# Kernel optimization log

Hardware: AMD Instinct MI355X
Metric: run time of the kernel (lower is better)

## Reference

```python
import jax, jax.numpy as jnp
import numpy as np

N, D, C, S, E, K, MIN_MATCH, N_ITER = 100000, 128, 16, 16, 3200000, 64, 1, 4


def setup_inputs() -> dict:
    key = jax.random.key(0)
    k1, k2, k3, k4 = jax.random.split(key, 4)
    es = jax.random.normal(k1, (N, D), jnp.float32)
    edge_index = jax.random.randint(k2, (2, E), 0, N)
    seeds = jax.random.randint(k3, (C, S), 0, N)
    W = jax.random.normal(k4, (D, D), jnp.float32) / np.float32(np.sqrt(D))
    return {"es": es, "edge_index": edge_index, "seeds": seeds, "W": W, "n_iter": N_ITER}


def _memory_step(es, idx, hx, W):
    # ragged gather of last expansion, padded to fixed size per class: [C, k, D]
    inp = es[idx]
    d = inp.shape[-1]
    q = jnp.mean(inp, axis=1) if hx is None else hx          # attention query [C, D]
    logits = jnp.einsum('ckd,cd->ck', inp, q) / jnp.sqrt(jnp.float32(d))
    a = jax.nn.softmax(logits, axis=-1)                      # [C, k]
    ctx = jnp.einsum('ck,ckd->cd', a, inp)                   # attended read [C, D]
    pre = ctx if hx is None else ctx + hx                    # recurrent memory update
    return jnp.tanh(pre @ W)                                 # [C, D]


def _cosine(x, y):
    xn = x / (jnp.linalg.norm(x, axis=-1, keepdims=True) + 1e-8)
    yn = y / (jnp.linalg.norm(y, axis=-1, keepdims=True) + 1e-8)
    return xn @ yn.T                                         # [N, C]


def _expand(es, W, edge_index, seeds, n_iter):
    n, c = es.shape[0], seeds.shape[0]
    src, dst = edge_index[0], edge_index[1]
    # known_mask.scatter_(0, seed_all, 1)
    known = jnp.zeros((n,), bool).at[seeds.ravel()].set(True)
    # get_cate_mask(seeds, N): per-class membership mask [C, N]
    cate = jnp.zeros((c, n), bool).at[jnp.arange(c)[:, None], seeds].set(True)
    hx, last = None, seeds
    outs, exps, hxes = [], [], []
    for _ in range(n_iter):
        hx = _memory_step(es, last, hx, W)
        # get_cate_neighbors: per-class count of in-edges whose source is in the class
        counts = jax.vmap(lambda m: jax.ops.segment_sum(m, dst, num_segments=n))(
            cate.astype(jnp.float32)[:, src])                # [C, N]
        valid = (counts >= MIN_MATCH) & (~known)[None, :]    # [C, N]
        scores = _cosine(es, hx).T                           # [C, N]
        # _select: top n_expansion valid nodes per class (finite fill avoids -inf grads)
        probs, idx = jax.lax.top_k(jnp.where(valid, scores, -1e9), K)
        known = known.at[idx.ravel()].set(True)
        cate = cate.at[jnp.arange(c)[:, None], idx].set(True)
        last = idx
        outs.append(probs); exps.append(idx); hxes.append(hx)
    return jnp.stack(outs), jnp.stack(exps), jnp.stack(hxes)


def reference(es, edge_index, seeds, W, n_iter):
    return _expand(es, W, edge_index, seeds, n_iter)
```

## Files before the change

kernel.cpp:

```cpp
#include <hip/hip_runtime.h>
#include <math.h>

#define NN 100000
#define DD 128
#define CC 16
#define SS 16
#define EE 3200000
#define KK 64
#define NIT 4
#define CNT_STRIDE 32
#define NB 32
#define SLMAX 4096
#define MM (NB * KK)
#define EB ((EE + 255) / 256)
#define INF_STAMP 0x7fffffff

typedef unsigned long long ull;

__device__ inline ull ordkey(double d) {
    long long b = __double_as_longlong(d);
    return (b < 0) ? ~(ull)b : ((ull)b | 0x8000000000000000ULL);
}
__device__ inline double keyord(ull u) {
    long long b = (u & 0x8000000000000000ULL)
                    ? (long long)(u & 0x7FFFFFFFFFFFFFFFULL)
                    : (long long)~u;
    return __longlong_as_double(b);
}
__device__ inline bool gt(ull ka, int na, ull kb, int nb) {
    return (ka > kb) || (ka == kb && na < nb);
}

__device__ inline void wsort64(ull& k, int& n, int lane) {
    for (int k2 = 2; k2 <= 64; k2 <<= 1) {
        for (int j = k2 >> 1; j; j >>= 1) {
            ull ok = __shfl_xor(k, j, 64);
            int on = __shfl_xor(n, j, 64);
            bool isLow = (lane & j) == 0;
            bool d = (k2 == 64) || ((lane & k2) == 0);
            bool wantMax = (d == isLow);
            if (wantMax == gt(ok, on, k, n)) { k = ok; n = on; }
        }
    }
}
__device__ inline void wmerge64(ull& k, int& n, int lane) {
    for (int j = 32; j; j >>= 1) {
        ull ok = __shfl_xor(k, j, 64);
        int on = __shfl_xor(n, j, 64);
        bool wantMax = (lane & j) == 0;
        if (wantMax == gt(ok, on, k, n)) { k = ok; n = on; }
    }
}


__global__ __launch_bounds__(256)
void k_init(const float* __restrict__ es, double* __restrict__ inv_norm,
            int* __restrict__ known, unsigned* __restrict__ cate,
            unsigned* __restrict__ nbr) {
    int wave = threadIdx.x >> 6, lane = threadIdx.x & 63;
    int n = blockIdx.x * 4 + wave;
    if (n >= NN) return;
    float a = es[(long)n * DD + lane];
    float b = es[(long)n * DD + 64 + lane];
    double p = (double)a * (double)a + (double)b * (double)b;
    for (int o = 32; o > 0; o >>= 1) p += __shfl_xor(p, o, 64);
    if (lane == 0) {
        inv_norm[n] = 1.0 / (sqrt(p) + 1e-8);
        known[n] = INF_STAMP;
        cate[n] = 0;
        nbr[n] = 0;
    }
}

__global__ void k_seed(const int* __restrict__ seeds, int* __restrict__ known,
                       unsigned* __restrict__ cate) {
    int i = threadIdx.x;
    if (i < CC * SS) {
        int n = seeds[i];
        known[n] = 0;
        atomicOr(&cate[n], 1u << (i / SS));
    }
}


__global__ __launch_bounds__(256)
void k_memedge(const float* __restrict__ es, const float* __restrict__ Wm,
               const int* __restrict__ seeds, const int* __restrict__ last,
               double* __restrict__ hx, double* __restrict__ hxn,
               float* __restrict__ out, int* __restrict__ cnt,
               const int* __restrict__ edge, const unsigned* __restrict__ cate,
               unsigned* __restrict__ nbr, int t) {
    __shared__ float  inp[KK][DD + 1];
    __shared__ int    rowS[KK];
    __shared__ double q[DD];
    __shared__ double lg[KK];
    __shared__ double sr[KK];
    __shared__ double pre[DD];
    __shared__ double red[DD];
    int tid = threadIdx.x;

    if (blockIdx.x >= CC) {
        long e = (long)(blockIdx.x - CC) * 256 + tid;
        if (e < EE) {
            int s = edge[e];
            unsigned m = cate[s];
            if (m) {
                int d = edge[EE + e];
                atomicOr(&nbr[d], m);
            }
        }
        return;
    }

    int c = blockIdx.x;
    if (tid == 0) cnt[c * CNT_STRIDE] = 0;
    int k = (t == 0) ? SS : KK;
    if (tid < KK) {
        lg[tid] = -1.0e308;
        if (tid < k) rowS[tid] = (t == 0) ? seeds[c * SS + tid] : last[c * KK + tid];
    }
    __syncthreads();
    for (int i = tid; i < k * DD; i += 256)
        inp[i >> 7][i & 127] = es[(long)rowS[i >> 7] * DD + (i & 127)];
    __syncthreads();
    if (tid < DD) {
        if (t == 0) {
            double s = 0;
            for (int j = 0; j < k; ++j) s += (double)inp[j][tid];
            q[tid] = s / (double)k;
        } else {
            q[tid] = hx[c * DD + tid];
        }
    }
    __syncthreads();
    if (tid < k) {
        double s = 0;
        for (int i = 0; i < DD; ++i) s += (double)inp[tid][i] * q[i];
        lg[tid] = s / sqrt((double)DD);
    }
    __syncthreads();
    if (tid < KK) sr[tid] = lg[tid];
    __syncthreads();
    for (int st = 32; st > 0; st >>= 1) {
        if (tid < st) sr[tid] = fmax(sr[tid], sr[tid + st]);
        __syncthreads();
    }
    double mx = sr[0];
    __syncthreads();
    if (tid < KK) {
        double e = (tid < k) ? exp(lg[tid] - mx) : 0.0;
        lg[tid] = e; sr[tid] = e;
    }
    __syncthreads();
    for (int st = 32; st > 0; st >>= 1) {
        if (tid < st) sr[tid] += sr[tid + st];
        __syncthreads();
    }
    double sm = sr[0];
    __syncthreads();
    if (tid < KK) lg[tid] /= sm;
    __syncthreads();
    if (tid < DD) {
        double ctx = 0;
        for (int j = 0; j < k; ++j) ctx += lg[j] * (double)inp[j][tid];
        pre[tid] = (t == 0) ? ctx : (ctx + q[tid]);
    }
    __syncthreads();
    double h = 0;
    if (tid < DD) {
        for (int i = 0; i < DD; ++i) h += pre[i] * (double)Wm[i * DD + tid];
        h = tanh(h);
        red[tid] = h * h;
    }
    __syncthreads();
    for (int st = 64; st > 0; st >>= 1) {
        if (tid < st) red[tid] += red[tid + st];
        __syncthreads();
    }
    if (tid < DD) {
        double inv = 1.0 / (sqrt(red[0]) + 1e-8);
        hx[c * DD + tid] = h;
        hxn[c * DD + tid] = h * inv;
        out[2 * NIT * CC * KK + t * CC * DD + c * DD + tid] = (float)h;
    }
}


__global__ __launch_bounds__(256)
void k_cand(const float* __restrict__ es, const double* __restrict__ inv_norm,
            const int* __restrict__ known, const unsigned* __restrict__ nbr,
            const double* __restrict__ hxn,
            int* __restrict__ cnt, int* __restrict__ cidx,
            ull* __restrict__ ckey, int cap, int t) {
    __shared__ int    pair[256 * 16];
    __shared__ short  prank[256 * 16];
    __shared__ double hxnL[CC * 129];
    __shared__ int    lcnt[CC];
    __shared__ int    base[CC];
    __shared__ int    npair;
    int tid = threadIdx.x;

    for (int i = tid; i < CC * DD; i += 256)
        hxnL[(i >> 7) * 129 + (i & 127)] = hxn[i];
    if (tid < CC) lcnt[tid] = 0;
    if (tid == 0) npair = 0;
    __syncthreads();

    int n = blockIdx.x * 256 + tid;
    unsigned m = 0;
    if (n < NN && known[n] > t) m = nbr[n];
    while (m) {
        int c = __ffs(m) - 1;
        m &= m - 1;
        int r = atomicAdd(&lcnt[c], 1);
        int p = atomicAdd(&npair, 1);
        pair[p] = (n << 4) | c;
        prank[p] = (short)r;
    }
    __syncthreads();

    if (tid < CC && lcnt[tid] > 0)
        base[tid] = atomicAdd(&cnt[tid * CNT_STRIDE], lcnt[tid]);
    __syncthreads();

    int np = npair;
    for (int t2 = tid; t2 < np; t2 += 256) {
        int pk = pair[t2];
        int nn = pk >> 4, c = pk & 15;
        const float4* row = (const float4*)(es + (long)nn * DD);
        const double* h = &hxnL[c * 129];
        double s = 0;
        #pragma unroll
        for (int i = 0; i < 32; ++i) {
            float4 v = row[i];
            s += (double)v.x * h[4 * i + 0] + (double)v.y * h[4 * i + 1]
               + (double)v.z * h[4 * i + 2] + (double)v.w * h[4 * i + 3];
        }
        int pos = base[c] + (int)prank[t2];
        if (pos < cap) {
            cidx[(long)c * cap + pos] = nn;
            ckey[(long)c * cap + pos] = ordkey(s * inv_norm[nn]);
        }
    }
}


__global__ __launch_bounds__(256)
void k_top(const int* __restrict__ cnt, const int* __restrict__ cidx,
           const ull* __restrict__ ckey, int cap,
           ull* __restrict__ tkey, int* __restrict__ tnode) {
    __shared__ ull ks[SLMAX];
    __shared__ int ns[SLMAX];
    int c = blockIdx.x / NB, b = blockIdx.x % NB;
    int tid = threadIdx.x, wave = tid >> 6, lane = tid & 63;
    int count = min(cnt[c * CNT_STRIDE], cap);
    int per = (count + NB - 1) / NB;
    int start = b * per;
    int m = min(per, count - start);
    int sl = 64;
    while (sl < per) sl <<= 1;
    int nruns = sl >> 6;
    for (int r = wave; r < nruns; r += 4) {
        int i = (r << 6) + lane;
        ull k; int n;
        if (i < m) { k = ckey[(long)c * cap + start + i]; n = cidx[(long)c * cap + start + i]; }
        else       { k = 0ULL; n = 0x7FFFFFFF; }
        wsort64(k, n, lane);
        ks[i] = k; ns[i] = n;
    }
    __syncthreads();
    for (int step = 1; step < nruns; step <<= 1) {
        int npair2 = nruns / (2 * step);
        for (int pr = wave; pr < npair2; pr += 4) {
            int ra = pr * 2 * step, rb = ra + step;
            ull ka = ks[(ra << 6) + lane];       int na = ns[(ra << 6) + lane];
            ull kb = ks[(rb << 6) + 63 - lane];  int nb2 = ns[(rb << 6) + 63 - lane];
            if (gt(kb, nb2, ka, na)) { ka = kb; na = nb2; }
            wmerge64(ka, na, lane);
            ks[(ra << 6) + lane] = ka; ns[(ra << 6) + lane] = na;
        }
        __syncthreads();
    }
    if (tid < KK) {
        tkey[(long)c * MM + b * KK + tid] = ks[tid];
        tnode[(long)c * MM + b * KK + tid] = ns[tid];
    }
}


__global__ __launch_bounds__(256)
void k_mergeupd(const int* __restrict__ cnt,
                const ull* __restrict__ tkey, const int* __restrict__ tnode,
                int* __restrict__ known, const unsigned* __restrict__ nbr,
                unsigned* __restrict__ cate, int* __restrict__ last,
                float* __restrict__ out, int cap, int t) {
    __shared__ ull ks[MM];
    __shared__ int ns[MM];
    int c = blockIdx.x, tid = threadIdx.x, wave = tid >> 6, lane = tid & 63;
    for (int i = tid; i < MM; i += 256) {
        ks[i] = tkey[(long)c * MM + i];
        ns[i] = tnode[(long)c * MM + i];
    }
    __syncthreads();
    for (int step = 1; step < NB; step <<= 1) {
        int npair2 = NB / (2 * step);
        for (int pr = wave; pr < npair2; pr += 4) {
            int ra = pr * 2 * step, rb = ra + step;
            ull ka = ks[(ra << 6) + lane];       int na = ns[(ra << 6) + lane];
            ull kb = ks[(rb << 6) + 63 - lane];  int nb2 = ns[(rb << 6) + 63 - lane];
            if (gt(kb, nb2, ka, na)) { ka = kb; na = nb2; }
            wmerge64(ka, na, lane);
            ks[(ra << 6) + lane] = ka; ns[(ra << 6) + lane] = na;
        }
        __syncthreads();
    }
    int count = min(cnt[c * CNT_STRIDE], cap);
    int nsel = min(count, KK);
    if (tid < KK && tid < nsel) {
        int n = ns[tid];
        out[t * CC * KK + c * KK + tid] = (float)keyord(ks[tid]);
        out[NIT * CC * KK + t * CC * KK + c * KK + tid] = (float)n;
        last[c * KK + tid] = n;
        known[n] = t + 1;
        atomicOr(&cate[n], 1u << c);
    }
    if (tid == 0 && nsel < KK) {
        int r = nsel;
        for (int n = 0; n < NN && r < KK; ++n) {
            bool valid = ((nbr[n] >> c) & 1u) && (known[n] > t);
            if (!valid) {
                out[t * CC * KK + c * KK + r] = -1e9f;
                out[NIT * CC * KK + t * CC * KK + c * KK + r] = (float)n;
                last[c * KK + r] = n;
                known[n] = t + 1;
                atomicOr(&cate[n], 1u << c);
                ++r;
            }
        }
    }
}


extern "C" void kernel_launch(void* const* d_in, const int* in_sizes, int n_in,
                              void* d_out, int out_size, void* d_ws, size_t ws_size,
                              hipStream_t stream) {
    const float* es    = (const float*)d_in[0];
    const int*   edge  = (const int*)d_in[1];
    const int*   seeds = (const int*)d_in[2];
    const float* W     = (const float*)d_in[3];
    float* out = (float*)d_out;

    char* p = (char*)d_ws;
    auto alloc = [&](size_t bytes) -> char* {
        char* r = p;
        p += (bytes + 255) & ~(size_t)255;
        return r;
    };
    double*   inv_norm = (double*)alloc((size_t)NN * 8);
    int*      known    = (int*)alloc((size_t)NN * 4);
    unsigned* cate     = (unsigned*)alloc((size_t)NN * 4);
    unsigned* nbr      = (unsigned*)alloc((size_t)NN * 4);
    double*   hx       = (double*)alloc(CC * DD * 8);
    double*   hxn      = (double*)alloc(CC * DD * 8);
    int*      last     = (int*)alloc(CC * KK * 4);
    int*      cnt      = (int*)alloc(CC * CNT_STRIDE * 4);
    ull*      tkey     = (ull*)alloc((size_t)CC * MM * 8);
    int*      tnode    = (int*)alloc((size_t)CC * MM * 4);
    size_t used = (size_t)(p - (char*)d_ws);
    size_t rem = (ws_size > used + 8192) ? (ws_size - used - 8192) : 0;
    long capl = (long)(rem / (CC * 12));
    if (capl > NN) capl = NN;
    if (capl < 1) capl = 1;
    int cap = (int)capl;
    int*    cidx = (int*)alloc((size_t)CC * cap * 4);
    ull*    ckey = (ull*)alloc((size_t)CC * cap * 8);

    k_init<<<(NN + 3) / 4, 256, 0, stream>>>(es, inv_norm, known, cate, nbr);
    k_seed<<<1, 256, 0, stream>>>(seeds, known, cate);

    for (int t = 0; t < NIT; ++t) {
        k_memedge<<<CC + EB, 256, 0, stream>>>(es, W, seeds, last, hx, hxn, out,
                                               cnt, edge, cate, nbr, t);
        k_cand<<<(NN + 255) / 256, 256, 0, stream>>>(es, inv_norm, known, nbr, hxn,
                                                     cnt, cidx, ckey, cap, t);
        k_top<<<CC * NB, 256, 0, stream>>>(cnt, cidx, ckey, cap, tkey, tnode);
        k_mergeupd<<<CC, 256, 0, stream>>>(cnt, tkey, tnode, known, nbr,
                                           cate, last, out, cap, t);
    }
}
```

Before: 308.4 us.

## Fuse all stages into one persistent kernel with software grid barriers

Replaces the per-iteration sequence of memory/edge, candidate, top-k and merge kernels with a single persistent kernel of 256 blocks that synchronises via an atomic generation-counter grid barrier. Init and seeding are merged into one pass that checks seed membership from shared memory. This removes many kernel launches and launch gaps. In exchange, it runs bandwidth-heavy edge and candidate passes with only one block per CU, which may reduce latency hiding, and it relies on all blocks being co-resident.

```diff
diff --git a/kernel.cpp b/kernel.cpp
--- a/kernel.cpp
+++ b/kernel.cpp
@@ -12,10 +12,30 @@
 #define NB 32
 #define SLMAX 4096
 #define MM (NB * KK)
-#define EB ((EE + 255) / 256)
+#define GRID 256
+#define NCHUNK ((NN + 255) / 256)
 #define INF_STAMP 0x7fffffff
 
 typedef unsigned long long ull;
+
+__device__ int g_cnt = 0;
+__device__ int g_gen = 0;
+
+__device__ __forceinline__ void gridbar() {
+    __syncthreads();
+    if (threadIdx.x == 0) {
+        int g = __hip_atomic_load(&g_gen, __ATOMIC_RELAXED, __HIP_MEMORY_SCOPE_AGENT);
+        int a = __hip_atomic_fetch_add(&g_cnt, 1, __ATOMIC_ACQ_REL, __HIP_MEMORY_SCOPE_AGENT);
+        if (a == GRID - 1) {
+            __hip_atomic_store(&g_cnt, 0, __ATOMIC_RELAXED, __HIP_MEMORY_SCOPE_AGENT);
+            __hip_atomic_fetch_add(&g_gen, 1, __ATOMIC_RELEASE, __HIP_MEMORY_SCOPE_AGENT);
+        } else {
+            while (__hip_atomic_load(&g_gen, __ATOMIC_ACQUIRE, __HIP_MEMORY_SCOPE_AGENT) == g)
+                __builtin_amdgcn_s_sleep(1);
+        }
+    }
+    __syncthreads();
+}
 
 __device__ inline ull ordkey(double d) {
     long long b = __double_as_longlong(d);
@@ -52,291 +72,273 @@
     }
 }
 
-
-__global__ __launch_bounds__(256)
-void k_init(const float* __restrict__ es, double* __restrict__ inv_norm,
-            int* __restrict__ known, unsigned* __restrict__ cate,
-            unsigned* __restrict__ nbr) {
-    int wave = threadIdx.x >> 6, lane = threadIdx.x & 63;
-    int n = blockIdx.x * 4 + wave;
-    if (n >= NN) return;
-    float a = es[(long)n * DD + lane];
-    float b = es[(long)n * DD + 64 + lane];
-    double p = (double)a * (double)a + (double)b * (double)b;
-    for (int o = 32; o > 0; o >>= 1) p += __shfl_xor(p, o, 64);
-    if (lane == 0) {
-        inv_norm[n] = 1.0 / (sqrt(p) + 1e-8);
-        known[n] = INF_STAMP;
-        cate[n] = 0;
-        nbr[n] = 0;
-    }
-}
-
-__global__ void k_seed(const int* __restrict__ seeds, int* __restrict__ known,
-                       unsigned* __restrict__ cate) {
-    int i = threadIdx.x;
-    if (i < CC * SS) {
-        int n = seeds[i];
-        known[n] = 0;
-        atomicOr(&cate[n], 1u << (i / SS));
-    }
-}
-
-
-__global__ __launch_bounds__(256)
-void k_memedge(const float* __restrict__ es, const float* __restrict__ Wm,
-               const int* __restrict__ seeds, const int* __restrict__ last,
-               double* __restrict__ hx, double* __restrict__ hxn,
-               float* __restrict__ out, int* __restrict__ cnt,
-               const int* __restrict__ edge, const unsigned* __restrict__ cate,
-               unsigned* __restrict__ nbr, int t) {
-    __shared__ float  inp[KK][DD + 1];
-    __shared__ int    rowS[KK];
-    __shared__ double q[DD];
-    __shared__ double lg[KK];
-    __shared__ double sr[KK];
-    __shared__ double pre[DD];
-    __shared__ double red[DD];
-    int tid = threadIdx.x;
-
-    if (blockIdx.x >= CC) {
-        long e = (long)(blockIdx.x - CC) * 256 + tid;
-        if (e < EE) {
-            int s = edge[e];
-            unsigned m = cate[s];
-            if (m) {
-                int d = edge[EE + e];
-                atomicOr(&nbr[d], m);
-            }
-        }
-        return;
-    }
-
-    int c = blockIdx.x;
-    if (tid == 0) cnt[c * CNT_STRIDE] = 0;
-    int k = (t == 0) ? SS : KK;
-    if (tid < KK) {
-        lg[tid] = -1.0e308;
-        if (tid < k) rowS[tid] = (t == 0) ? seeds[c * SS + tid] : last[c * KK + tid];
-    }
+union SMem {
+    struct {
+        float inp[KK][DD + 1];
+        int rowS[KK];
+        double q[DD], lg[KK], sr[KK], pre[DD], red[DD];
+    } m;
+    struct {
+        int pair[256 * 16];
+        short prank[256 * 16];
+        double hxnL[CC * 129];
+        int lcnt[CC], base[CC], npair;
+    } cd;
+    struct { ull ks[SLMAX]; int ns[SLMAX]; } tp;
+    struct { int sn[CC * SS]; } sd;
+};
+
+__global__ __launch_bounds__(256, 1)
+void k_all(const float* __restrict__ es, const int* __restrict__ edge,
+           const int* __restrict__ seeds, const float* __restrict__ Wm,
+           float* __restrict__ out,
+           double* __restrict__ inv_norm, int* __restrict__ known,
+           unsigned* __restrict__ cate, unsigned* __restrict__ nbr,
+           double* __restrict__ hx, double* __restrict__ hxn,
+           int* __restrict__ last, int* __restrict__ cnt,
+           ull* __restrict__ tkey, int* __restrict__ tnode,
+           int* __restrict__ cidx, ull* __restrict__ ckey, int cap) {
+    __shared__ SMem sm;
+    int tid = threadIdx.x, wave = tid >> 6, lane = tid & 63;
+
+    if (tid < CC * SS) sm.sd.sn[tid] = seeds[tid];
     __syncthreads();
-    for (int i = tid; i < k * DD; i += 256)
-        inp[i >> 7][i & 127] = es[(long)rowS[i >> 7] * DD + (i & 127)];
-    __syncthreads();
-    if (tid < DD) {
-        if (t == 0) {
-            double s = 0;
-            for (int j = 0; j < k; ++j) s += (double)inp[j][tid];
-            q[tid] = s / (double)k;
+    for (int n = blockIdx.x * 4 + wave; n < NN; n += GRID * 4) {
+        float a = es[(long)n * DD + lane];
+        float b = es[(long)n * DD + 64 + lane];
+        double p = (double)a * (double)a + (double)b * (double)b;
+        for (int o = 32; o > 0; o >>= 1) p += __shfl_xor(p, o, 64);
+        unsigned bits = 0;
+        #pragma unroll
+        for (int j = 0; j < 4; ++j) {
+            int idx = lane * 4 + j;
+            if (sm.sd.sn[idx] == n) bits |= 1u << (idx >> 4);
+        }
+        for (int o = 32; o > 0; o >>= 1) bits |= __shfl_xor(bits, o, 64);
+        if (lane == 0) {
+            inv_norm[n] = 1.0 / (sqrt(p) + 1e-8);
+            known[n] = bits ? 0 : INF_STAMP;
+            cate[n] = bits;
+            nbr[n] = 0;
+        }
+    }
+    gridbar();
+
+    for (int t = 0; t < NIT; ++t) {
+        if (blockIdx.x < CC) {
+            int c = blockIdx.x;
+            if (tid == 0) cnt[c * CNT_STRIDE] = 0;
+            int k = (t == 0) ? SS : KK;
+            if (tid < KK) {
+                sm.m.lg[tid] = -1.0e308;
+                if (tid < k) sm.m.rowS[tid] = (t == 0) ? seeds[c * SS + tid]
+                                                       : last[c * KK + tid];
+            }
+            __syncthreads();
+            for (int i = tid; i < k * DD; i += 256)
+                sm.m.inp[i >> 7][i & 127] = es[(long)sm.m.rowS[i >> 7] * DD + (i & 127)];
+            __syncthreads();
+            if (tid < DD) {
+                if (t == 0) {
+                    double s = 0;
+                    for (int j = 0; j < k; ++j) s += (double)sm.m.inp[j][tid];
+                    sm.m.q[tid] = s / (double)k;
+                } else {
+                    sm.m.q[tid] = hx[c * DD + tid];
+                }
+            }
+            __syncthreads();
+            if (tid < k) {
+                double s = 0;
+                for (int i = 0; i < DD; ++i) s += (double)sm.m.inp[tid][i] * sm.m.q[i];
+                sm.m.lg[tid] = s / sqrt((double)DD);
+            }
+            __syncthreads();
+            if (tid < KK) sm.m.sr[tid] = sm.m.lg[tid];
+            __syncthreads();
+            for (int st = 32; st > 0; st >>= 1) {
+                if (tid < st) sm.m.sr[tid] = fmax(sm.m.sr[tid], sm.m.sr[tid + st]);
+                __syncthreads();
+            }
+            double mx = sm.m.sr[0];
+            __syncthreads();
+            if (tid < KK) {
+                double e = (tid < k) ? exp(sm.m.lg[tid] - mx) : 0.0;
+                sm.m.lg[tid] = e; sm.m.sr[tid] = e;
+            }
+            __syncthreads();
+            for (int st = 32; st > 0; st >>= 1) {
+                if (tid < st) sm.m.sr[tid] += sm.m.sr[tid + st];
+                __syncthreads();
+            }
+            double smm = sm.m.sr[0];
+            __syncthreads();
+            if (tid < KK) sm.m.lg[tid] /= smm;
+            __syncthreads();
+            if (tid < DD) {
+                double ctx = 0;
+                for (int j = 0; j < k; ++j) ctx += sm.m.lg[j] * (double)sm.m.inp[j][tid];
+                sm.m.pre[tid] = (t == 0) ? ctx : (ctx + sm.m.q[tid]);
+            }
+            __syncthreads();
+            double h = 0;
+            if (tid < DD) {
+                for (int i = 0; i < DD; ++i) h += sm.m.pre[i] * (double)Wm[i * DD + tid];
+                h = tanh(h);
+                sm.m.red[tid] = h * h;
+            }
+            __syncthreads();
+            for (int st = 64; st > 0; st >>= 1) {
+                if (tid < st) sm.m.red[tid] += sm.m.red[tid + st];
+                __syncthreads();
+            }
+            if (tid < DD) {
+                double inv = 1.0 / (sqrt(sm.m.red[0]) + 1e-8);
+                hx[c * DD + tid] = h;
+                hxn[c * DD + tid] = h * inv;
+                out[2 * NIT * CC * KK + t * CC * DD + c * DD + tid] = (float)h;
+            }
         } else {
-            q[tid] = hx[c * DD + tid];
-        }
-    }
-    __syncthreads();
-    if (tid < k) {
-        double s = 0;
-        for (int i = 0; i < DD; ++i) s += (double)inp[tid][i] * q[i];
-        lg[tid] = s / sqrt((double)DD);
-    }
-    __syncthreads();
-    if (tid < KK) sr[tid] = lg[tid];
-    __syncthreads();
-    for (int st = 32; st > 0; st >>= 1) {
-        if (tid < st) sr[tid] = fmax(sr[tid], sr[tid + st]);
+            const int stripe = (EE + (GRID - CC) - 1) / (GRID - CC);
+            long e0 = (long)(blockIdx.x - CC) * stripe;
+            long e1 = e0 + stripe; if (e1 > EE) e1 = EE;
+            for (long e = e0 + tid; e < e1; e += 256) {
+                int s = edge[e];
+                unsigned mm = cate[s];
+                if (mm) atomicOr(&nbr[edge[EE + e]], mm);
+            }
+        }
+        gridbar();
+
+        for (int i = tid; i < CC * DD; i += 256)
+            sm.cd.hxnL[(i >> 7) * 129 + (i & 127)] = hxn[i];
         __syncthreads();
-    }
-    double mx = sr[0];
-    __syncthreads();
-    if (tid < KK) {
-        double e = (tid < k) ? exp(lg[tid] - mx) : 0.0;
-        lg[tid] = e; sr[tid] = e;
-    }
-    __syncthreads();
-    for (int st = 32; st > 0; st >>= 1) {
-        if (tid < st) sr[tid] += sr[tid + st];
-        __syncthreads();
-    }
-    double sm = sr[0];
-    __syncthreads();
-    if (tid < KK) lg[tid] /= sm;
-    __syncthreads();
-    if (tid < DD) {
-        double ctx = 0;
-        for (int j = 0; j < k; ++j) ctx += lg[j] * (double)inp[j][tid];
-        pre[tid] = (t == 0) ? ctx : (ctx + q[tid]);
-    }
-    __syncthreads();
-    double h = 0;
-    if (tid < DD) {
-        for (int i = 0; i < DD; ++i) h += pre[i] * (double)Wm[i * DD + tid];
-        h = tanh(h);
-        red[tid] = h * h;
-    }
-    __syncthreads();
-    for (int st = 64; st > 0; st >>= 1) {
-        if (tid < st) red[tid] += red[tid + st];
-        __syncthreads();
-    }
-    if (tid < DD) {
-        double inv = 1.0 / (sqrt(red[0]) + 1e-8);
-        hx[c * DD + tid] = h;
-        hxn[c * DD + tid] = h * inv;
-        out[2 * NIT * CC * KK + t * CC * DD + c * DD + tid] = (float)h;
-    }
-}
-
-
-__global__ __launch_bounds__(256)
-void k_cand(const float* __restrict__ es, const double* __restrict__ inv_norm,
-            const int* __restrict__ known, const unsigned* __restrict__ nbr,
-            const double* __restrict__ hxn,
-            int* __restrict__ cnt, int* __restrict__ cidx,
-            ull* __restrict__ ckey, int cap, int t) {
-    __shared__ int    pair[256 * 16];
-    __shared__ short  prank[256 * 16];
-    __shared__ double hxnL[CC * 129];
-    __shared__ int    lcnt[CC];
-    __shared__ int    base[CC];
-    __shared__ int    npair;
-    int tid = threadIdx.x;
-
-    for (int i = tid; i < CC * DD; i += 256)
-        hxnL[(i >> 7) * 129 + (i & 127)] = hxn[i];
-    if (tid < CC) lcnt[tid] = 0;
-    if (tid == 0) npair = 0;
-    __syncthreads();
-
-    int n = blockIdx.x * 256 + tid;
-    unsigned m = 0;
-    if (n < NN && known[n] > t) m = nbr[n];
-    while (m) {
-        int c = __ffs(m) - 1;
-        m &= m - 1;
-        int r = atomicAdd(&lcnt[c], 1);
-        int p = atomicAdd(&npair, 1);
-        pair[p] = (n << 4) | c;
-        prank[p] = (short)r;
-    }
-    __syncthreads();
-
-    if (tid < CC && lcnt[tid] > 0)
-        base[tid] = atomicAdd(&cnt[tid * CNT_STRIDE], lcnt[tid]);
-    __syncthreads();
-
-    int np = npair;
-    for (int t2 = tid; t2 < np; t2 += 256) {
-        int pk = pair[t2];
-        int nn = pk >> 4, c = pk & 15;
-        const float4* row = (const float4*)(es + (long)nn * DD);
-        const double* h = &hxnL[c * 129];
-        double s = 0;
-        #pragma unroll
-        for (int i = 0; i < 32; ++i) {
-            float4 v = row[i];
-            s += (double)v.x * h[4 * i + 0] + (double)v.y * h[4 * i + 1]
-               + (double)v.z * h[4 * i + 2] + (double)v.w * h[4 * i + 3];
-        }
-        int pos = base[c] + (int)prank[t2];
-        if (pos < cap) {
-            cidx[(long)c * cap + pos] = nn;
-            ckey[(long)c * cap + pos] = ordkey(s * inv_norm[nn]);
-        }
-    }
-}
-
-
-__global__ __launch_bounds__(256)
-void k_top(const int* __restrict__ cnt, const int* __restrict__ cidx,
-           const ull* __restrict__ ckey, int cap,
-           ull* __restrict__ tkey, int* __restrict__ tnode) {
-    __shared__ ull ks[SLMAX];
-    __shared__ int ns[SLMAX];
-    int c = blockIdx.x / NB, b = blockIdx.x % NB;
-    int tid = threadIdx.x, wave = tid >> 6, lane = tid & 63;
-    int count = min(cnt[c * CNT_STRIDE], cap);
-    int per = (count + NB - 1) / NB;
-    int start = b * per;
-    int m = min(per, count - start);
-    int sl = 64;
-    while (sl < per) sl <<= 1;
-    int nruns = sl >> 6;
-    for (int r = wave; r < nruns; r += 4) {
-        int i = (r << 6) + lane;
-        ull k; int n;
-        if (i < m) { k = ckey[(long)c * cap + start + i]; n = cidx[(long)c * cap + start + i]; }
-        else       { k = 0ULL; n = 0x7FFFFFFF; }
-        wsort64(k, n, lane);
-        ks[i] = k; ns[i] = n;
-    }
-    __syncthreads();
-    for (int step = 1; step < nruns; step <<= 1) {
-        int npair2 = nruns / (2 * step);
-        for (int pr = wave; pr < npair2; pr += 4) {
-            int ra = pr * 2 * step, rb = ra + step;
-            ull ka = ks[(ra << 6) + lane];       int na = ns[(ra << 6) + lane];
-            ull kb = ks[(rb << 6) + 63 - lane];  int nb2 = ns[(rb << 6) + 63 - lane];
-            if (gt(kb, nb2, ka, na)) { ka = kb; na = nb2; }
-            wmerge64(ka, na, lane);
-            ks[(ra << 6) + lane] = ka; ns[(ra << 6) + lane] = na;
-        }
-        __syncthreads();
-    }
-    if (tid < KK) {
-        tkey[(long)c * MM + b * KK + tid] = ks[tid];
-        tnode[(long)c * MM + b * KK + tid] = ns[tid];
-    }
-}
-
-
-__global__ __launch_bounds__(256)
-void k_mergeupd(const int* __restrict__ cnt,
-                const ull* __restrict__ tkey, const int* __restrict__ tnode,
-                int* __restrict__ known, const unsigned* __restrict__ nbr,
-                unsigned* __restrict__ cate, int* __restrict__ last,
-                float* __restrict__ out, int cap, int t) {
-    __shared__ ull ks[MM];
-    __shared__ int ns[MM];
-    int c = blockIdx.x, tid = threadIdx.x, wave = tid >> 6, lane = tid & 63;
-    for (int i = tid; i < MM; i += 256) {
-        ks[i] = tkey[(long)c * MM + i];
-        ns[i] = tnode[(long)c * MM + i];
-    }
-    __syncthreads();
-    for (int step = 1; step < NB; step <<= 1) {
-        int npair2 = NB / (2 * step);
-        for (int pr = wave; pr < npair2; pr += 4) {
-            int ra = pr * 2 * step, rb = ra + step;
-            ull ka = ks[(ra << 6) + lane];       int na = ns[(ra << 6) + lane];
-            ull kb = ks[(rb << 6) + 63 - lane];  int nb2 = ns[(rb << 6) + 63 - lane];
-            if (gt(kb, nb2, ka, na)) { ka = kb; na = nb2; }
-            wmerge64(ka, na, lane);
-            ks[(ra << 6) + lane] = ka; ns[(ra << 6) + lane] = na;
-        }
-        __syncthreads();
-    }
-    int count = min(cnt[c * CNT_STRIDE], cap);
-    int nsel = min(count, KK);
-    if (tid < KK && tid < nsel) {
-        int n = ns[tid];
-        out[t * CC * KK + c * KK + tid] = (float)keyord(ks[tid]);
-        out[NIT * CC * KK + t * CC * KK + c * KK + tid] = (float)n;
-        last[c * KK + tid] = n;
-        known[n] = t + 1;
-        atomicOr(&cate[n], 1u << c);
-    }
-    if (tid == 0 && nsel < KK) {
-        int r = nsel;
-        for (int n = 0; n < NN && r < KK; ++n) {
-            bool valid = ((nbr[n] >> c) & 1u) && (known[n] > t);
-            if (!valid) {
-                out[t * CC * KK + c * KK + r] = -1e9f;
-                out[NIT * CC * KK + t * CC * KK + c * KK + r] = (float)n;
-                last[c * KK + r] = n;
+        for (int vb = blockIdx.x; vb < NCHUNK; vb += GRID) {
+            if (tid < CC) sm.cd.lcnt[tid] = 0;
+            if (tid == 0) sm.cd.npair = 0;
+            __syncthreads();
+            int n = vb * 256 + tid;
+            unsigned m = 0;
+            if (n < NN && known[n] > t) m = nbr[n];
+            while (m) {
+                int c = __ffs(m) - 1;
+                m &= m - 1;
+                int r = atomicAdd(&sm.cd.lcnt[c], 1);
+                int p = atomicAdd(&sm.cd.npair, 1);
+                sm.cd.pair[p] = (n << 4) | c;
+                sm.cd.prank[p] = (short)r;
+            }
+            __syncthreads();
+            if (tid < CC && sm.cd.lcnt[tid] > 0)
+                sm.cd.base[tid] = atomicAdd(&cnt[tid * CNT_STRIDE], sm.cd.lcnt[tid]);
+            __syncthreads();
+            int np = sm.cd.npair;
+            for (int t2 = tid; t2 < np; t2 += 256) {
+                int pk = sm.cd.pair[t2];
+                int nn = pk >> 4, c = pk & 15;
+                const float4* row = (const float4*)(es + (long)nn * DD);
+                const double* h = &sm.cd.hxnL[c * 129];
+                double s = 0;
+                #pragma unroll
+                for (int i = 0; i < 32; ++i) {
+                    float4 v = row[i];
+                    s += (double)v.x * h[4 * i + 0] + (double)v.y * h[4 * i + 1]
+                       + (double)v.z * h[4 * i + 2] + (double)v.w * h[4 * i + 3];
+                }
+                int pos = sm.cd.base[c] + (int)sm.cd.prank[t2];
+                if (pos < cap) {
+                    cidx[(long)c * cap + pos] = nn;
+                    ckey[(long)c * cap + pos] = ordkey(s * inv_norm[nn]);
+                }
+            }
+            __syncthreads();
+        }
+        gridbar();
+
+        for (int vt = blockIdx.x; vt < CC * NB; vt += GRID) {
+            int c = vt / NB, b = vt % NB;
+            int count = min(cnt[c * CNT_STRIDE], cap);
+            int per = (count + NB - 1) / NB;
+            int start = b * per;
+            int m2 = min(per, count - start);
+            int sl = 64;
+            while (sl < per) sl <<= 1;
+            int nruns = sl >> 6;
+            __syncthreads();
+            for (int r = wave; r < nruns; r += 4) {
+                int i = (r << 6) + lane;
+                ull k; int n;
+                if (i < m2) { k = ckey[(long)c * cap + start + i];
+                              n = cidx[(long)c * cap + start + i]; }
+                else        { k = 0ULL; n = 0x7FFFFFFF; }
+                wsort64(k, n, lane);
+                sm.tp.ks[i] = k; sm.tp.ns[i] = n;
+            }
+            __syncthreads();
+            for (int step = 1; step < nruns; step <<= 1) {
+                int npair2 = nruns / (2 * step);
+                for (int pr = wave; pr < npair2; pr += 4) {
+                    int ra = pr * 2 * step, rb = ra + step;
+                    ull ka = sm.tp.ks[(ra << 6) + lane];       int na = sm.tp.ns[(ra << 6) + lane];
+                    ull kb = sm.tp.ks[(rb << 6) + 63 - lane];  int nb2 = sm.tp.ns[(rb << 6) + 63 - lane];
+                    if (gt(kb, nb2, ka, na)) { ka = kb; na = nb2; }
+                    wmerge64(ka, na, lane);
+                    sm.tp.ks[(ra << 6) + lane] = ka; sm.tp.ns[(ra << 6) + lane] = na;
+                }
+                __syncthreads();
+            }
+            if (tid < KK) {
+                tkey[(long)c * MM + b * KK + tid] = sm.tp.ks[tid];
+                tnode[(long)c * MM + b * KK + tid] = sm.tp.ns[tid];
+            }
+        }
+        gridbar();
+
+        if (blockIdx.x < CC) {
+            int c = blockIdx.x;
+            for (int i = tid; i < MM; i += 256) {
+                sm.tp.ks[i] = tkey[(long)c * MM + i];
+                sm.tp.ns[i] = tnode[(long)c * MM + i];
+            }
+            __syncthreads();
+            for (int step = 1; step < NB; step <<= 1) {
+                int npair2 = NB / (2 * step);
+                for (int pr = wave; pr < npair2; pr += 4) {
+                    int ra = pr * 2 * step, rb = ra + step;
+                    ull ka = sm.tp.ks[(ra << 6) + lane];       int na = sm.tp.ns[(ra << 6) + lane];
+                    ull kb = sm.tp.ks[(rb << 6) + 63 - lane];  int nb2 = sm.tp.ns[(rb << 6) + 63 - lane];
+                    if (gt(kb, nb2, ka, na)) { ka = kb; na = nb2; }
+                    wmerge64(ka, na, lane);
+                    sm.tp.ks[(ra << 6) + lane] = ka; sm.tp.ns[(ra << 6) + lane] = na;
+                }
+                __syncthreads();
+            }
+            int count = min(cnt[c * CNT_STRIDE], cap);
+            int nsel = min(count, KK);
+            if (tid < KK && tid < nsel) {
+                int n = sm.tp.ns[tid];
+                out[t * CC * KK + c * KK + tid] = (float)keyord(sm.tp.ks[tid]);
+                out[NIT * CC * KK + t * CC * KK + c * KK + tid] = (float)n;
+                last[c * KK + tid] = n;
                 known[n] = t + 1;
                 atomicOr(&cate[n], 1u << c);
-                ++r;
-            }
-        }
+            }
+            if (tid == 0 && nsel < KK) {
+                int r = nsel;
+                for (int n = 0; n < NN && r < KK; ++n) {
+                    bool valid = ((nbr[n] >> c) & 1u) && (known[n] > t);
+                    if (!valid) {
+                        out[t * CC * KK + c * KK + r] = -1e9f;
+                        out[NIT * CC * KK + t * CC * KK + c * KK + r] = (float)n;
+                        last[c * KK + r] = n;
+                        known[n] = t + 1;
+                        atomicOr(&cate[n], 1u << c);
+                        ++r;
+                    }
+                }
+            }
+        }
+        gridbar();
     }
 }
 
@@ -375,16 +377,7 @@
     int*    cidx = (int*)alloc((size_t)CC * cap * 4);
     ull*    ckey = (ull*)alloc((size_t)CC * cap * 8);
 
-    k_init<<<(NN + 3) / 4, 256, 0, stream>>>(es, inv_norm, known, cate, nbr);
-    k_seed<<<1, 256, 0, stream>>>(seeds, known, cate);
-
-    for (int t = 0; t < NIT; ++t) {
-        k_memedge<<<CC + EB, 256, 0, stream>>>(es, W, seeds, last, hx, hxn, out,
-                                               cnt, edge, cate, nbr, t);
-        k_cand<<<(NN + 255) / 256, 256, 0, stream>>>(es, inv_norm, known, nbr, hxn,
-                                                     cnt, cidx, ckey, cap, t);
-        k_top<<<CC * NB, 256, 0, stream>>>(cnt, cidx, ckey, cap, tkey, tnode);
-        k_mergeupd<<<CC, 256, 0, stream>>>(cnt, tkey, tnode, known, nbr,
-                                           cate, last, out, cap, t);
-    }
-}
+    k_all<<<GRID, 256, 0, stream>>>(es, edge, seeds, W, out,
+                                    inv_norm, known, cate, nbr, hx, hxn,
+                                    last, cnt, tkey, tnode, cidx, ckey, cap);
+}
```

Result: slower. 971.0 us (+214.9%).

## Fuse top-k sort and merge into one kernel with last-block-done reduction

Applied to the files above, without the earlier changes.

Replaces the two-kernel top-k (per-block sort into shared memory, then per-class merge kernel) with a single kernel. Each wave streams its slice of candidates and folds them into a running 64-wide top list held in registers. The last block of each class, found through an atomic done counter, does the final fold and the update. Seed initialization is folded into k_init, and the k_cand pair packing drops the separate rank array. This removes kernel launches and large shared-memory sorts, but the final merge is serialized through one wave per class and relies on acq_rel atomic ordering.

```diff
diff --git a/kernel.cpp b/kernel.cpp
--- a/kernel.cpp
+++ b/kernel.cpp
@@ -9,9 +9,9 @@
 #define KK 64
 #define NIT 4
 #define CNT_STRIDE 32
-#define NB 32
-#define SLMAX 4096
-#define MM (NB * KK)
+#define RUNS 64
+#define CHUNK 256
+#define NCH ((NN + CHUNK - 1) / CHUNK)
 #define EB ((EE + 255) / 256)
 #define INF_STAMP 0x7fffffff
 
@@ -51,34 +51,40 @@
         if (wantMax == gt(ok, on, k, n)) { k = ok; n = on; }
     }
 }
+__device__ inline void wfold(ull& ak, int& an, ull k, int n, int lane) {
+    ull rk = __shfl(k, 63 - lane, 64);
+    int rn = __shfl(n, 63 - lane, 64);
+    if (gt(rk, rn, ak, an)) { ak = rk; an = rn; }
+    wmerge64(ak, an, lane);
+}
 
 
 __global__ __launch_bounds__(256)
-void k_init(const float* __restrict__ es, double* __restrict__ inv_norm,
-            int* __restrict__ known, unsigned* __restrict__ cate,
-            unsigned* __restrict__ nbr) {
-    int wave = threadIdx.x >> 6, lane = threadIdx.x & 63;
+void k_init(const float* __restrict__ es, const int* __restrict__ seeds,
+            double* __restrict__ inv_norm, int* __restrict__ known,
+            unsigned* __restrict__ cate, unsigned* __restrict__ nbr) {
+    __shared__ int sn[CC * SS];
+    int tid = threadIdx.x, wave = tid >> 6, lane = tid & 63;
+    if (tid < CC * SS) sn[tid] = seeds[tid];
+    __syncthreads();
     int n = blockIdx.x * 4 + wave;
     if (n >= NN) return;
     float a = es[(long)n * DD + lane];
     float b = es[(long)n * DD + 64 + lane];
     double p = (double)a * (double)a + (double)b * (double)b;
     for (int o = 32; o > 0; o >>= 1) p += __shfl_xor(p, o, 64);
+    unsigned bits = 0;
+    #pragma unroll
+    for (int j = 0; j < 4; ++j) {
+        int idx = lane * 4 + j;
+        if (sn[idx] == n) bits |= 1u << (idx >> 4);
+    }
+    for (int o = 32; o > 0; o >>= 1) bits |= __shfl_xor(bits, o, 64);
     if (lane == 0) {
         inv_norm[n] = 1.0 / (sqrt(p) + 1e-8);
-        known[n] = INF_STAMP;
-        cate[n] = 0;
+        known[n] = bits ? 0 : INF_STAMP;
+        cate[n] = bits;
         nbr[n] = 0;
-    }
-}
-
-__global__ void k_seed(const int* __restrict__ seeds, int* __restrict__ known,
-                       unsigned* __restrict__ cate) {
-    int i = threadIdx.x;
-    if (i < CC * SS) {
-        int n = seeds[i];
-        known[n] = 0;
-        atomicOr(&cate[n], 1u << (i / SS));
     }
 }
 
@@ -87,16 +93,12 @@
 void k_memedge(const float* __restrict__ es, const float* __restrict__ Wm,
                const int* __restrict__ seeds, const int* __restrict__ last,
                double* __restrict__ hx, double* __restrict__ hxn,
-               float* __restrict__ out, int* __restrict__ cnt,
+               float* __restrict__ out, int* __restrict__ cnt, int* __restrict__ done,
                const int* __restrict__ edge, const unsigned* __restrict__ cate,
                unsigned* __restrict__ nbr, int t) {
     __shared__ float  inp[KK][DD + 1];
     __shared__ int    rowS[KK];
-    __shared__ double q[DD];
-    __shared__ double lg[KK];
-    __shared__ double sr[KK];
-    __shared__ double pre[DD];
-    __shared__ double red[DD];
+    __shared__ double q[DD], lg[KK], sr[KK], pre[DD], red[DD];
     int tid = threadIdx.x;
 
     if (blockIdx.x >= CC) {
@@ -104,16 +106,13 @@
         if (e < EE) {
             int s = edge[e];
             unsigned m = cate[s];
-            if (m) {
-                int d = edge[EE + e];
-                atomicOr(&nbr[d], m);
-            }
+            if (m) atomicOr(&nbr[edge[EE + e]], m);
         }
         return;
     }
 
     int c = blockIdx.x;
-    if (tid == 0) cnt[c * CNT_STRIDE] = 0;
+    if (tid == 0) { cnt[c * CNT_STRIDE] = 0; done[c * CNT_STRIDE] = 0; }
     int k = (t == 0) ? SS : KK;
     if (tid < KK) {
         lg[tid] = -1.0e308;
@@ -192,12 +191,9 @@
             const double* __restrict__ hxn,
             int* __restrict__ cnt, int* __restrict__ cidx,
             ull* __restrict__ ckey, int cap, int t) {
-    __shared__ int    pair[256 * 16];
-    __shared__ short  prank[256 * 16];
+    __shared__ int    pair[CHUNK * CC];
     __shared__ double hxnL[CC * 129];
-    __shared__ int    lcnt[CC];
-    __shared__ int    base[CC];
-    __shared__ int    npair;
+    __shared__ int    lcnt[CC], base[CC], npair;
     int tid = threadIdx.x;
 
     for (int i = tid; i < CC * DD; i += 256)
@@ -206,7 +202,7 @@
     if (tid == 0) npair = 0;
     __syncthreads();
 
-    int n = blockIdx.x * 256 + tid;
+    int n = blockIdx.x * CHUNK + tid;
     unsigned m = 0;
     if (n < NN && known[n] > t) m = nbr[n];
     while (m) {
@@ -214,8 +210,7 @@
         m &= m - 1;
         int r = atomicAdd(&lcnt[c], 1);
         int p = atomicAdd(&npair, 1);
-        pair[p] = (n << 4) | c;
-        prank[p] = (short)r;
+        pair[p] = (tid << 12) | (r << 4) | c;
     }
     __syncthreads();
 
@@ -226,7 +221,8 @@
     int np = npair;
     for (int t2 = tid; t2 < np; t2 += 256) {
         int pk = pair[t2];
-        int nn = pk >> 4, c = pk & 15;
+        int c = pk & 15, r = (pk >> 4) & 255, ln = pk >> 12;
+        int nn = blockIdx.x * CHUNK + ln;
         const float4* row = (const float4*)(es + (long)nn * DD);
         const double* h = &hxnL[c * 129];
         double s = 0;
@@ -236,7 +232,7 @@
             s += (double)v.x * h[4 * i + 0] + (double)v.y * h[4 * i + 1]
                + (double)v.z * h[4 * i + 2] + (double)v.w * h[4 * i + 3];
         }
-        int pos = base[c] + (int)prank[t2];
+        int pos = base[c] + r;
         if (pos < cap) {
             cidx[(long)c * cap + pos] = nn;
             ckey[(long)c * cap + pos] = ordkey(s * inv_norm[nn]);
@@ -246,95 +242,67 @@
 
 
 __global__ __launch_bounds__(256)
-void k_top(const int* __restrict__ cnt, const int* __restrict__ cidx,
-           const ull* __restrict__ ckey, int cap,
-           ull* __restrict__ tkey, int* __restrict__ tnode) {
-    __shared__ ull ks[SLMAX];
-    __shared__ int ns[SLMAX];
-    int c = blockIdx.x / NB, b = blockIdx.x % NB;
-    int tid = threadIdx.x, wave = tid >> 6, lane = tid & 63;
-    int count = min(cnt[c * CNT_STRIDE], cap);
-    int per = (count + NB - 1) / NB;
-    int start = b * per;
-    int m = min(per, count - start);
-    int sl = 64;
-    while (sl < per) sl <<= 1;
-    int nruns = sl >> 6;
-    for (int r = wave; r < nruns; r += 4) {
-        int i = (r << 6) + lane;
-        ull k; int n;
-        if (i < m) { k = ckey[(long)c * cap + start + i]; n = cidx[(long)c * cap + start + i]; }
-        else       { k = 0ULL; n = 0x7FFFFFFF; }
-        wsort64(k, n, lane);
-        ks[i] = k; ns[i] = n;
-    }
-    __syncthreads();
-    for (int step = 1; step < nruns; step <<= 1) {
-        int npair2 = nruns / (2 * step);
-        for (int pr = wave; pr < npair2; pr += 4) {
-            int ra = pr * 2 * step, rb = ra + step;
-            ull ka = ks[(ra << 6) + lane];       int na = ns[(ra << 6) + lane];
-            ull kb = ks[(rb << 6) + 63 - lane];  int nb2 = ns[(rb << 6) + 63 - lane];
-            if (gt(kb, nb2, ka, na)) { ka = kb; na = nb2; }
-            wmerge64(ka, na, lane);
-            ks[(ra << 6) + lane] = ka; ns[(ra << 6) + lane] = na;
-        }
-        __syncthreads();
-    }
-    if (tid < KK) {
-        tkey[(long)c * MM + b * KK + tid] = ks[tid];
-        tnode[(long)c * MM + b * KK + tid] = ns[tid];
-    }
-}
-
-
-__global__ __launch_bounds__(256)
-void k_mergeupd(const int* __restrict__ cnt,
-                const ull* __restrict__ tkey, const int* __restrict__ tnode,
+void k_topmerge(const int* __restrict__ cnt, const int* __restrict__ cidx,
+                const ull* __restrict__ ckey, int* __restrict__ done,
+                ull* __restrict__ tkey, int* __restrict__ tnode,
                 int* __restrict__ known, const unsigned* __restrict__ nbr,
                 unsigned* __restrict__ cate, int* __restrict__ last,
                 float* __restrict__ out, int cap, int t) {
-    __shared__ ull ks[MM];
-    __shared__ int ns[MM];
-    int c = blockIdx.x, tid = threadIdx.x, wave = tid >> 6, lane = tid & 63;
-    for (int i = tid; i < MM; i += 256) {
-        ks[i] = tkey[(long)c * MM + i];
-        ns[i] = tnode[(long)c * MM + i];
-    }
-    __syncthreads();
-    for (int step = 1; step < NB; step <<= 1) {
-        int npair2 = NB / (2 * step);
-        for (int pr = wave; pr < npair2; pr += 4) {
-            int ra = pr * 2 * step, rb = ra + step;
-            ull ka = ks[(ra << 6) + lane];       int na = ns[(ra << 6) + lane];
-            ull kb = ks[(rb << 6) + 63 - lane];  int nb2 = ns[(rb << 6) + 63 - lane];
-            if (gt(kb, nb2, ka, na)) { ka = kb; na = nb2; }
-            wmerge64(ka, na, lane);
-            ks[(ra << 6) + lane] = ka; ns[(ra << 6) + lane] = na;
-        }
-        __syncthreads();
-    }
+    __shared__ int win;
+    int tid = threadIdx.x, wave = tid >> 6, lane = tid & 63;
+    int c = blockIdx.x >> 4;
+    int w = (blockIdx.x & 15) * 4 + wave;
     int count = min(cnt[c * CNT_STRIDE], cap);
-    int nsel = min(count, KK);
-    if (tid < KK && tid < nsel) {
-        int n = ns[tid];
-        out[t * CC * KK + c * KK + tid] = (float)keyord(ks[tid]);
-        out[NIT * CC * KK + t * CC * KK + c * KK + tid] = (float)n;
-        last[c * KK + tid] = n;
-        known[n] = t + 1;
-        atomicOr(&cate[n], 1u << c);
-    }
-    if (tid == 0 && nsel < KK) {
-        int r = nsel;
-        for (int n = 0; n < NN && r < KK; ++n) {
-            bool valid = ((nbr[n] >> c) & 1u) && (known[n] > t);
-            if (!valid) {
-                out[t * CC * KK + c * KK + r] = -1e9f;
-                out[NIT * CC * KK + t * CC * KK + c * KK + r] = (float)n;
-                last[c * KK + r] = n;
-                known[n] = t + 1;
-                atomicOr(&cate[n], 1u << c);
-                ++r;
+    int per = (count + RUNS - 1) / RUNS;
+    int lo = w * per, hi = min(count, lo + per);
+    ull ak = 0ULL; int an = 0x7FFFFFFF;
+    for (int bs = lo; bs < hi; bs += 64) {
+        int idx = bs + lane;
+        ull k; int n;
+        if (idx < hi) { k = ckey[(long)c * cap + idx]; n = cidx[(long)c * cap + idx]; }
+        else          { k = 0ULL; n = 0x7FFFFFFF; }
+        wsort64(k, n, lane);
+        wfold(ak, an, k, n, lane);
+    }
+    tkey[((long)c * RUNS + w) * 64 + lane] = ak;
+    tnode[((long)c * RUNS + w) * 64 + lane] = an;
+    __syncthreads();
+    if (tid == 0) {
+        int prev = __hip_atomic_fetch_add(&done[c * CNT_STRIDE], 1,
+                                          __ATOMIC_ACQ_REL, __HIP_MEMORY_SCOPE_AGENT);
+        win = (prev == 15);
+    }
+    __syncthreads();
+    if (!win) return;
+
+    if (wave == 0) {
+        ull fk = 0ULL; int fn = 0x7FFFFFFF;
+        for (int r = 0; r < RUNS; ++r) {
+            ull k = tkey[((long)c * RUNS + r) * 64 + lane];
+            int n = tnode[((long)c * RUNS + r) * 64 + lane];
+            wfold(fk, fn, k, n, lane);
+        }
+        int nsel = min(count, KK);
+        if (lane < nsel) {
+            int n = fn;
+            out[t * CC * KK + c * KK + lane] = (float)keyord(fk);
+            out[NIT * CC * KK + t * CC * KK + c * KK + lane] = (float)n;
+            last[c * KK + lane] = n;
+            known[n] = t + 1;
+            atomicOr(&cate[n], 1u << c);
+        }
+        if (lane == 0 && nsel < KK) {
+            int r = nsel;
+            for (int n = 0; n < NN && r < KK; ++n) {
+                bool valid = ((nbr[n] >> c) & 1u) && (known[n] > t);
+                if (!valid) {
+                    out[t * CC * KK + c * KK + r] = -1e9f;
+                    out[NIT * CC * KK + t * CC * KK + c * KK + r] = (float)n;
+                    last[c * KK + r] = n;
+                    known[n] = t + 1;
+                    atomicOr(&cate[n], 1u << c);
+                    ++r;
+                }
             }
         }
     }
@@ -364,8 +332,9 @@
     double*   hxn      = (double*)alloc(CC * DD * 8);
     int*      last     = (int*)alloc(CC * KK * 4);
     int*      cnt      = (int*)alloc(CC * CNT_STRIDE * 4);
-    ull*      tkey     = (ull*)alloc((size_t)CC * MM * 8);
-    int*      tnode    = (int*)alloc((size_t)CC * MM * 4);
+    int*      done     = (int*)alloc(CC * CNT_STRIDE * 4);
+    ull*      tkey     = (ull*)alloc((size_t)CC * RUNS * 64 * 8);
+    int*      tnode    = (int*)alloc((size_t)CC * RUNS * 64 * 4);
     size_t used = (size_t)(p - (char*)d_ws);
     size_t rem = (ws_size > used + 8192) ? (ws_size - used - 8192) : 0;
     long capl = (long)(rem / (CC * 12));
@@ -375,16 +344,14 @@
     int*    cidx = (int*)alloc((size_t)CC * cap * 4);
     ull*    ckey = (ull*)alloc((size_t)CC * cap * 8);
 
-    k_init<<<(NN + 3) / 4, 256, 0, stream>>>(es, inv_norm, known, cate, nbr);
-    k_seed<<<1, 256, 0, stream>>>(seeds, known, cate);
+    k_init<<<(NN + 3) / 4, 256, 0, stream>>>(es, seeds, inv_norm, known, cate, nbr);
 
     for (int t = 0; t < NIT; ++t) {
         k_memedge<<<CC + EB, 256, 0, stream>>>(es, W, seeds, last, hx, hxn, out,
-                                               cnt, edge, cate, nbr, t);
-        k_cand<<<(NN + 255) / 256, 256, 0, stream>>>(es, inv_norm, known, nbr, hxn,
-                                                     cnt, cidx, ckey, cap, t);
-        k_top<<<CC * NB, 256, 0, stream>>>(cnt, cidx, ckey, cap, tkey, tnode);
-        k_mergeupd<<<CC, 256, 0, stream>>>(cnt, tkey, tnode, known, nbr,
-                                           cate, last, out, cap, t);
-    }
-}
+                                               cnt, done, edge, cate, nbr, t);
+        k_cand<<<NCH, 256, 0, stream>>>(es, inv_norm, known, nbr, hxn,
+                                        cnt, cidx, ckey, cap, t);
+        k_topmerge<<<CC * 16, 256, 0, stream>>>(cnt, cidx, ckey, done, tkey, tnode,
+                                                known, nbr, cate, last, out, cap, t);
+    }
+}
```

Measured after the change: 479.3 us. 55.4% more time.
